# Performance work log

Hardware: AMD Instinct MI355X
Metric: run time of the kernel (lower is better)

## Reference

```python
import jax, jax.numpy as jnp
import numpy as np

N_NODES = 100000
N_EDGES = 1600000
D_IN, D_HID, D_OUT = 32, 64, 32


def gcn_conv(x, src, dst, W, b, n_nodes):
    """PyG-style GCNConv: x @ W, add self-loops, symmetric deg^-1/2 norm, scatter-add, + bias."""
    h = x @ W  # [N, d_out]
    ones = jnp.ones(src.shape[0], dtype=h.dtype)
    # in-degree at dst, +1 for the implicit self-loop
    deg = jax.ops.segment_sum(ones, dst, num_segments=n_nodes) + 1.0  # [N]
    dinv_sqrt = jax.lax.rsqrt(deg)
    norm = dinv_sqrt[src] * dinv_sqrt[dst]  # [E]
    agg = jax.ops.segment_sum(h[src] * norm[:, None], dst, num_segments=n_nodes)  # [N, d_out]
    agg = agg + h * (dinv_sqrt * dinv_sqrt)[:, None]  # self-loop term: deg^-1 * h_i
    return agg + b


def setup_inputs() -> dict:
    key = jax.random.key(0)
    ks = jax.random.split(key, 5)
    x = jax.random.normal(ks[0], (N_NODES, D_IN), dtype=jnp.float32)
    edge_index = jax.random.randint(ks[1], (2, N_EDGES), 0, N_NODES, dtype=jnp.int64)
    # Glorot-ish init for GCN weights
    W1 = jax.random.normal(ks[2], (D_IN, D_HID), dtype=jnp.float32) * (1.0 / np.sqrt(D_IN))
    b1 = jnp.zeros((D_HID,), dtype=jnp.float32)
    W2 = jax.random.normal(ks[3], (D_HID, D_OUT), dtype=jnp.float32) * (1.0 / np.sqrt(D_HID))
    b2 = jnp.zeros((D_OUT,), dtype=jnp.float32)
    return {"x": x, "edge_index": edge_index, "W1": W1, "b1": b1, "W2": W2, "b2": b2}


def reference(x, edge_index, W1, b1, W2, b2):
    src, dst = edge_index[0], edge_index[1]
    h = jax.nn.relu(gcn_conv(x, src, dst, W1, b1, N_NODES))
    h = gcn_conv(h, src, dst, W2, b2, N_NODES)
    # per-edge score: gather-multiply-sum
    logits = jnp.sum(h[src] * h[dst], axis=-1)  # [E]
    return logits
```

## Files before the change

kernel.cpp:

```cpp
#include <hip/hip_runtime.h>
#include <hip/hip_fp16.h>

#define N_NODES 100000
#define N_EDGES 1600000
#define D_IN 32
#define D_HID 64
#define D_OUT 32
#define CAP 48
#define PGROUPS 250
#define PGSIZE 400
#define PBINCAP 7200
#define PTILE 8192

__global__ void __launch_bounds__(512) partition_kernel(
    const int* __restrict__ src, const int* __restrict__ dst,
    int* __restrict__ gcur, int2* __restrict__ bins, int E) {
    __shared__ int lcnt[PGROUPS];
    __shared__ int lbase[PGROUPS];
    for (int t = threadIdx.x; t < PGROUPS; t += 512) lcnt[t] = 0;
    __syncthreads();
    int base = blockIdx.x * PTILE + threadIdx.x * 16;
    int s[16], d[16], g[16], p[16];
    int nloc = 0;
    if (base < E) nloc = min(16, E - base);
    if (nloc == 16) {
#pragma unroll
        for (int q = 0; q < 4; ++q) {
            int4 sv = *(const int4*)(src + base + 4 * q);
            int4 dv = *(const int4*)(dst + base + 4 * q);
            s[4*q+0] = sv.x; s[4*q+1] = sv.y; s[4*q+2] = sv.z; s[4*q+3] = sv.w;
            d[4*q+0] = dv.x; d[4*q+1] = dv.y; d[4*q+2] = dv.z; d[4*q+3] = dv.w;
        }
#pragma unroll
        for (int k = 0; k < 16; ++k) {
            g[k] = d[k] / PGSIZE;
            p[k] = atomicAdd(&lcnt[g[k]], 1);
        }
    } else {
        for (int k = 0; k < nloc; ++k) { s[k] = src[base + k]; d[k] = dst[base + k]; }
        for (int k = 0; k < nloc; ++k) {
            g[k] = d[k] / PGSIZE;
            p[k] = atomicAdd(&lcnt[g[k]], 1);
        }
    }
    __syncthreads();
    for (int t = threadIdx.x; t < PGROUPS; t += 512)
        lbase[t] = lcnt[t] ? atomicAdd(&gcur[t], lcnt[t]) : 0;
    __syncthreads();
    if (nloc == 16) {
#pragma unroll
        for (int k = 0; k < 16; ++k) {
            int idx = lbase[g[k]] + p[k];
            if (idx < PBINCAP) bins[(size_t)g[k] * PBINCAP + idx] = make_int2(s[k], d[k]);
        }
    } else {
        for (int k = 0; k < nloc; ++k) {
            int idx = lbase[g[k]] + p[k];
            if (idx < PBINCAP) bins[(size_t)g[k] * PBINCAP + idx] = make_int2(s[k], d[k]);
        }
    }
}

__global__ void __launch_bounds__(256) sort_scale_kernel(
    const int2* __restrict__ bins, const int* __restrict__ gcur,
    const float* __restrict__ x,
    int* __restrict__ cnt, int* __restrict__ csr, __half* __restrict__ xd) {
    __shared__ int lcnt[PGSIZE];
    int g = blockIdx.x;
    for (int t = threadIdx.x; t < PGSIZE; t += 256) lcnt[t] = 0;
    __syncthreads();
    int n = gcur[g];
    if (n > PBINCAP) n = PBINCAP;
    const int2* bin = bins + (size_t)g * PBINCAP;
    int lo = g * PGSIZE;
    int i = threadIdx.x;
    for (; i + 768 < n; i += 1024) {
        int2 e0 = bin[i];
        int2 e1 = bin[i + 256];
        int2 e2 = bin[i + 512];
        int2 e3 = bin[i + 768];
        int p0 = atomicAdd(&lcnt[e0.y - lo], 1);
        int p1 = atomicAdd(&lcnt[e1.y - lo], 1);
        int p2 = atomicAdd(&lcnt[e2.y - lo], 1);
        int p3 = atomicAdd(&lcnt[e3.y - lo], 1);
        if (p0 < CAP) csr[(size_t)e0.y * CAP + p0] = e0.x;
        if (p1 < CAP) csr[(size_t)e1.y * CAP + p1] = e1.x;
        if (p2 < CAP) csr[(size_t)e2.y * CAP + p2] = e2.x;
        if (p3 < CAP) csr[(size_t)e3.y * CAP + p3] = e3.x;
    }
    for (; i < n; i += 256) {
        int2 e = bin[i];
        int pos = atomicAdd(&lcnt[e.y - lo], 1);
        if (pos < CAP) csr[(size_t)e.y * CAP + pos] = e.x;
    }
    __syncthreads();
    for (int t = threadIdx.x; t < PGSIZE; t += 256) cnt[lo + t] = lcnt[t];
    for (int u = threadIdx.x; u < PGSIZE * 8; u += 256) {
        int t = u >> 3, c = (u & 7) * 4;
        int node = lo + t;
        float di = rsqrtf((float)lcnt[t] + 1.0f);
        float4 v = *(const float4*)(x + (size_t)node * D_IN + c);
        __half2 h0 = __floats2half2_rn(v.x * di, v.y * di);
        __half2 h1 = __floats2half2_rn(v.z * di, v.w * di);
        float2 packed = make_float2(*(float*)&h0, *(float*)&h1);
        *(float2*)(xd + (size_t)node * D_IN + c) = packed;
    }
}

#define ACC2(acc, raw) do { __half2* hp_ = (__half2*)&(raw); \
    float2 g0_ = __half22float2(hp_[0]), g1_ = __half22float2(hp_[1]); \
    (acc).x += g0_.x; (acc).y += g0_.y; (acc).z += g1_.x; (acc).w += g1_.y; } while (0)

__global__ void __launch_bounds__(256) agg1_kernel(
    const int* __restrict__ cnt, const int* __restrict__ csr,
    const __half* __restrict__ xd, float* __restrict__ axf, int N) {
    int gid = blockIdx.x * 256 + threadIdx.x;
    int n = gid >> 3;
    int c = (gid & 7) * 4;
    int cn = cnt[n];
    int m = cn < CAP ? cn : CAP;
    float di = rsqrtf((float)cn + 1.0f);

    float4 acc, accB = make_float4(0.f, 0.f, 0.f, 0.f);
    {
        float2 raw = *(const float2*)(xd + (size_t)n * D_IN + c);
        __half2* hp = (__half2*)&raw;
        float2 f0 = __half22float2(hp[0]), f1 = __half22float2(hp[1]);
        acc = make_float4(f0.x, f0.y, f1.x, f1.y);
    }
    const int4* row4 = (const int4*)(csr + (size_t)n * CAP);
    int i = 0;
    for (; i + 8 <= m; i += 8) {
        int4 sa = row4[(i >> 2) + 0];
        int4 sb = row4[(i >> 2) + 1];
        float2 r0 = *(const float2*)(xd + (size_t)sa.x * D_IN + c);
        float2 r1 = *(const float2*)(xd + (size_t)sa.y * D_IN + c);
        float2 r2 = *(const float2*)(xd + (size_t)sa.z * D_IN + c);
        float2 r3 = *(const float2*)(xd + (size_t)sa.w * D_IN + c);
        float2 r4 = *(const float2*)(xd + (size_t)sb.x * D_IN + c);
        float2 r5 = *(const float2*)(xd + (size_t)sb.y * D_IN + c);
        float2 r6 = *(const float2*)(xd + (size_t)sb.z * D_IN + c);
        float2 r7 = *(const float2*)(xd + (size_t)sb.w * D_IN + c);
        ACC2(acc, r0); ACC2(accB, r1); ACC2(acc, r2); ACC2(accB, r3);
        ACC2(acc, r4); ACC2(accB, r5); ACC2(acc, r6); ACC2(accB, r7);
    }
    for (; i + 4 <= m; i += 4) {
        int4 s4 = row4[i >> 2];
        float2 r0 = *(const float2*)(xd + (size_t)s4.x * D_IN + c);
        float2 r1 = *(const float2*)(xd + (size_t)s4.y * D_IN + c);
        float2 r2 = *(const float2*)(xd + (size_t)s4.z * D_IN + c);
        float2 r3 = *(const float2*)(xd + (size_t)s4.w * D_IN + c);
        ACC2(acc, r0); ACC2(accB, r1); ACC2(acc, r2); ACC2(accB, r3);
    }
    const int* row = csr + (size_t)n * CAP;
    for (; i < m; ++i) {
        float2 raw = *(const float2*)(xd + (size_t)row[i] * D_IN + c);
        ACC2(acc, raw);
    }
    float4 o = make_float4(di * (acc.x + accB.x), di * (acc.y + accB.y),
                           di * (acc.z + accB.z), di * (acc.w + accB.w));
    *(float4*)(axf + (size_t)n * D_IN + c) = o;
}

__global__ void __launch_bounds__(256) mlp_kernel(
    const int* __restrict__ cnt, const float* __restrict__ axf,
    const float* __restrict__ W1, const float* __restrict__ b1,
    const float* __restrict__ W2, __half* __restrict__ g2, int N) {
    __shared__ float W1s[D_IN * D_HID];
    __shared__ float W2s[D_HID * D_OUT];
    __shared__ float b1s[D_HID];
    __shared__ float axs[32][36];
    __shared__ float h1s[32][65];
    for (int t = threadIdx.x; t < D_IN * D_HID; t += 256) W1s[t] = W1[t];
    for (int t = threadIdx.x; t < D_HID * D_OUT; t += 256) W2s[t] = W2[t];
    if (threadIdx.x < D_HID) b1s[threadIdx.x] = b1[threadIdx.x];

    int nl = threadIdx.x >> 3;
    int l8 = threadIdx.x & 7;
    int n = blockIdx.x * 32 + nl;
    int c = l8 * 4;
    float di = rsqrtf((float)cnt[n] + 1.0f);
    float4 av = *(const float4*)(axf + (size_t)n * D_IN + c);
    *(float4*)&axs[nl][c] = av;
    __syncthreads();

#pragma unroll
    for (int jj = 0; jj < 8; ++jj) {
        int j = l8 * 8 + jj;
        float a = b1s[j];
#pragma unroll
        for (int k = 0; k < D_IN; ++k) a += axs[nl][k] * W1s[k * D_HID + j];
        h1s[nl][j] = fmaxf(a, 0.f);
    }
    __syncthreads();

    float o0 = 0.f, o1 = 0.f, o2 = 0.f, o3 = 0.f;
#pragma unroll
    for (int k = 0; k < D_HID; ++k) {
        float hk = h1s[nl][k];
        o0 += hk * W2s[k * D_OUT + c + 0];
        o1 += hk * W2s[k * D_OUT + c + 1];
        o2 += hk * W2s[k * D_OUT + c + 2];
        o3 += hk * W2s[k * D_OUT + c + 3];
    }
    __half2 p0 = __floats2half2_rn(di * o0, di * o1);
    __half2 p1 = __floats2half2_rn(di * o2, di * o3);
    float2 packed = make_float2(*(float*)&p0, *(float*)&p1);
    *(float2*)(g2 + (size_t)n * D_OUT + c) = packed;
}

__global__ void __launch_bounds__(256) agg2_kernel(
    const int* __restrict__ cnt, const int* __restrict__ csr,
    const __half* __restrict__ G, const float* __restrict__ b,
    __half* __restrict__ OUT, int N) {
    long long gid = (long long)blockIdx.x * blockDim.x + threadIdx.x;
    int n = (int)(gid >> 3);
    int c = ((int)gid & 7) * 4;
    if (n >= N) return;
    int cn = cnt[n];
    int m = cn < CAP ? cn : CAP;
    float4 acc, accB = make_float4(0.f, 0.f, 0.f, 0.f);
    {
        float2 raw = *(const float2*)(G + (long long)n * D_OUT + c);
        __half2* hp = (__half2*)&raw;
        float2 f0 = __half22float2(hp[0]), f1 = __half22float2(hp[1]);
        acc = make_float4(f0.x, f0.y, f1.x, f1.y);
    }
    const int4* row4 = (const int4*)(csr + (long long)n * CAP);
    int i = 0;
    for (; i + 8 <= m; i += 8) {
        int4 sa = row4[(i >> 2) + 0];
        int4 sb = row4[(i >> 2) + 1];
        float2 r0 = *(const float2*)(G + (long long)sa.x * D_OUT + c);
        float2 r1 = *(const float2*)(G + (long long)sa.y * D_OUT + c);
        float2 r2 = *(const float2*)(G + (long long)sa.z * D_OUT + c);
        float2 r3 = *(const float2*)(G + (long long)sa.w * D_OUT + c);
        float2 r4 = *(const float2*)(G + (long long)sb.x * D_OUT + c);
        float2 r5 = *(const float2*)(G + (long long)sb.y * D_OUT + c);
        float2 r6 = *(const float2*)(G + (long long)sb.z * D_OUT + c);
        float2 r7 = *(const float2*)(G + (long long)sb.w * D_OUT + c);
        ACC2(acc, r0); ACC2(accB, r1); ACC2(acc, r2); ACC2(accB, r3);
        ACC2(acc, r4); ACC2(accB, r5); ACC2(acc, r6); ACC2(accB, r7);
    }
    for (; i + 4 <= m; i += 4) {
        int4 s4 = row4[i >> 2];
        float2 r0 = *(const float2*)(G + (long long)s4.x * D_OUT + c);
        float2 r1 = *(const float2*)(G + (long long)s4.y * D_OUT + c);
        float2 r2 = *(const float2*)(G + (long long)s4.z * D_OUT + c);
        float2 r3 = *(const float2*)(G + (long long)s4.w * D_OUT + c);
        ACC2(acc, r0); ACC2(accB, r1); ACC2(acc, r2); ACC2(accB, r3);
    }
    const int* row = csr + (long long)n * CAP;
    for (; i < m; ++i) {
        float2 raw = *(const float2*)(G + (long long)row[i] * D_OUT + c);
        ACC2(acc, raw);
    }
    float di = rsqrtf((float)cn + 1.0f);
    __half2 h0 = __floats2half2_rn(di * (acc.x + accB.x) + b[c + 0],
                                   di * (acc.y + accB.y) + b[c + 1]);
    __half2 h1 = __floats2half2_rn(di * (acc.z + accB.z) + b[c + 2],
                                   di * (acc.w + accB.w) + b[c + 3]);
    float2 packed = make_float2(*(float*)&h0, *(float*)&h1);
    *(float2*)(OUT + (long long)n * D_OUT + c) = packed;
}

__global__ void logits_kernel(const int* __restrict__ src, const int* __restrict__ dst,
                              const __half* __restrict__ H, float* __restrict__ out, int E) {
    long long gid = (long long)blockIdx.x * blockDim.x + threadIdx.x;
    int e = (int)(gid >> 2);
    int c = ((int)gid & 3) * 8;
    if (e >= E) return;
    int s = src[e], d = dst[e];
    float4 ra = *(const float4*)(H + (long long)s * D_OUT + c);
    float4 rb = *(const float4*)(H + (long long)d * D_OUT + c);
    __half2* pa = (__half2*)&ra;
    __half2* pb = (__half2*)&rb;
    float p = 0.f;
#pragma unroll
    for (int k = 0; k < 4; ++k) {
        float2 fa = __half22float2(pa[k]);
        float2 fb = __half22float2(pb[k]);
        p += fa.x * fb.x + fa.y * fb.y;
    }
    p += __shfl_xor(p, 1);
    p += __shfl_xor(p, 2);
    if ((gid & 3) == 0) out[e] = p;
}

extern "C" void kernel_launch(void* const* d_in, const int* in_sizes, int n_in,
                              void* d_out, int out_size, void* d_ws, size_t ws_size,
                              hipStream_t stream) {
    const float* x  = (const float*)d_in[0];
    const int* edge = (const int*)d_in[1];
    const float* W1 = (const float*)d_in[2];
    const float* b1 = (const float*)d_in[3];
    const float* W2 = (const float*)d_in[4];
    const float* b2 = (const float*)d_in[5];
    float* out = (float*)d_out;

    const int* src = edge;
    const int* dst = edge + N_EDGES;

    char* ws = (char*)d_ws;
    int*    gcur = (int*)ws;
    int*    cnt  = gcur + 256;
    int*    csr  = cnt + N_NODES;
    int2*   bins = (int2*)(csr + (size_t)N_NODES * CAP);
    __half* xd   = (__half*)(bins + (size_t)PGROUPS * PBINCAP);
    float*  axf  = (float*)bins;
    __half* g2h  = xd;
    __half* h2h  = (__half*)bins;

    hipMemsetAsync(gcur, 0, 256 * sizeof(int), stream);

    partition_kernel<<<(N_EDGES + PTILE - 1) / PTILE, 512, 0, stream>>>(src, dst, gcur, bins, N_EDGES);

    sort_scale_kernel<<<PGROUPS, 256, 0, stream>>>(bins, gcur, x, cnt, csr, xd);

    agg1_kernel<<<(N_NODES * 8) / 256, 256, 0, stream>>>(cnt, csr, xd, axf, N_NODES);

    mlp_kernel<<<N_NODES / 32, 256, 0, stream>>>(cnt, axf, W1, b1, W2, g2h, N_NODES);

    agg2_kernel<<<(N_NODES * 8 + 255) / 256, 256, 0, stream>>>(cnt, csr, g2h, b2, h2h, N_NODES);

    logits_kernel<<<(N_EDGES * 4) / 256, 256, 0, stream>>>(src, dst, h2h, out, N_EDGES);
}
```

Baseline: 217.8 us.

## Split node feature tables into two 16-column planes processed in separate passes

Stores the scaled input features, hidden aggregates, layer-2 projections and final embeddings as two planes of 16 channels each instead of interleaved 32-channel rows. Each aggregation and the edge-logit kernel now run twice, once per plane, with the second logit pass accumulating into the output. The intent is to halve the working set each gather pass touches so it fits better in L2/MALL cache during random neighbor gathers. The cost is re-reading the CSR indices and edge lists twice, extra launches, and a read-modify-write of the output.

```diff
diff --git a/kernel.cpp b/kernel.cpp
--- a/kernel.cpp
+++ b/kernel.cpp
@@ -6,6 +6,7 @@
 #define D_IN 32
 #define D_HID 64
 #define D_OUT 32
+#define PL 16
 #define CAP 48
 #define PGROUPS 250
 #define PGSIZE 400
@@ -103,7 +104,8 @@
         __half2 h0 = __floats2half2_rn(v.x * di, v.y * di);
         __half2 h1 = __floats2half2_rn(v.z * di, v.w * di);
         float2 packed = make_float2(*(float*)&h0, *(float*)&h1);
-        *(float2*)(xd + (size_t)node * D_IN + c) = packed;
+        __half* xp = xd + (size_t)(c >> 4) * N_NODES * PL;
+        *(float2*)(xp + (size_t)node * PL + (c & 15)) = packed;
     }
 }
 
@@ -111,19 +113,20 @@
     float2 g0_ = __half22float2(hp_[0]), g1_ = __half22float2(hp_[1]); \
     (acc).x += g0_.x; (acc).y += g0_.y; (acc).z += g1_.x; (acc).w += g1_.y; } while (0)
 
-__global__ void __launch_bounds__(256) agg1_kernel(
+__global__ void __launch_bounds__(256) agg1_plane_kernel(
     const int* __restrict__ cnt, const int* __restrict__ csr,
-    const __half* __restrict__ xd, float* __restrict__ axf, int N) {
+    const __half* __restrict__ xdp, float* __restrict__ axfp, int N) {
     int gid = blockIdx.x * 256 + threadIdx.x;
-    int n = gid >> 3;
-    int c = (gid & 7) * 4;
+    int n = gid >> 2;
+    int c = (gid & 3) * 4;
+    if (n >= N) return;
     int cn = cnt[n];
     int m = cn < CAP ? cn : CAP;
     float di = rsqrtf((float)cn + 1.0f);
 
     float4 acc, accB = make_float4(0.f, 0.f, 0.f, 0.f);
     {
-        float2 raw = *(const float2*)(xd + (size_t)n * D_IN + c);
+        float2 raw = *(const float2*)(xdp + (size_t)n * PL + c);
         __half2* hp = (__half2*)&raw;
         float2 f0 = __half22float2(hp[0]), f1 = __half22float2(hp[1]);
         acc = make_float4(f0.x, f0.y, f1.x, f1.y);
@@ -133,33 +136,34 @@
     for (; i + 8 <= m; i += 8) {
         int4 sa = row4[(i >> 2) + 0];
         int4 sb = row4[(i >> 2) + 1];
-        float2 r0 = *(const float2*)(xd + (size_t)sa.x * D_IN + c);
-        float2 r1 = *(const float2*)(xd + (size_t)sa.y * D_IN + c);
-        float2 r2 = *(const float2*)(xd + (size_t)sa.z * D_IN + c);
-        float2 r3 = *(const float2*)(xd + (size_t)sa.w * D_IN + c);
-        float2 r4 = *(const float2*)(xd + (size_t)sb.x * D_IN + c);
-        float2 r5 = *(const float2*)(xd + (size_t)sb.y * D_IN + c);
-        float2 r6 = *(const float2*)(xd + (size_t)sb.z * D_IN + c);
-        float2 r7 = *(const float2*)(xd + (size_t)sb.w * D_IN + c);
+        float2 r0 = *(const float2*)(xdp + (size_t)sa.x * PL + c);
+        float2 r1 = *(const float2*)(xdp + (size_t)sa.y * PL + c);
+        float2 r2 = *(const float2*)(xdp + (size_t)sa.z * PL + c);
+        float2 r3 = *(const float2*)(xdp + (size_t)sa.w * PL + c);
+        float2 r4 = *(const float2*)(xdp + (size_t)sb.x * PL + c);
+        float2 r5 = *(const float2*)(xdp + (size_t)sb.y * PL + c);
+        float2 r6 = *(const float2*)(xdp + (size_t)sb.z * PL + c);
+        float2 r7 = *(const float2*)(xdp + (size_t)sb.w * PL + c);
         ACC2(acc, r0); ACC2(accB, r1); ACC2(acc, r2); ACC2(accB, r3);
         ACC2(acc, r4); ACC2(accB, r5); ACC2(acc, r6); ACC2(accB, r7);
     }
     for (; i + 4 <= m; i += 4) {
         int4 s4 = row4[i >> 2];
-        float2 r0 = *(const float2*)(xd + (size_t)s4.x * D_IN + c);
-        float2 r1 = *(const float2*)(xd + (size_t)s4.y * D_IN + c);
-        float2 r2 = *(const float2*)(xd + (size_t)s4.z * D_IN + c);
-        float2 r3 = *(const float2*)(xd + (size_t)s4.w * D_IN + c);
+        float2 r0 = *(const float2*)(xdp + (size_t)s4.x * PL + c);
+        float2 r1 = *(const float2*)(xdp + (size_t)s4.y * PL + c);
+        float2 r2 = *(const float2*)(xdp + (size_t)s4.z * PL + c);
+        float2 r3 = *(const float2*)(xdp + (size_t)s4.w * PL + c);
         ACC2(acc, r0); ACC2(accB, r1); ACC2(acc, r2); ACC2(accB, r3);
     }
     const int* row = csr + (size_t)n * CAP;
     for (; i < m; ++i) {
-        float2 raw = *(const float2*)(xd + (size_t)row[i] * D_IN + c);
+        int sv = row[i];
+        float2 raw = *(const float2*)(xdp + (size_t)sv * PL + c);
         ACC2(acc, raw);
     }
     float4 o = make_float4(di * (acc.x + accB.x), di * (acc.y + accB.y),
                            di * (acc.z + accB.z), di * (acc.w + accB.w));
-    *(float4*)(axf + (size_t)n * D_IN + c) = o;
+    *(float4*)(axfp + (size_t)n * PL + c) = o;
 }
 
 __global__ void __launch_bounds__(256) mlp_kernel(
@@ -180,7 +184,8 @@
     int n = blockIdx.x * 32 + nl;
     int c = l8 * 4;
     float di = rsqrtf((float)cnt[n] + 1.0f);
-    float4 av = *(const float4*)(axf + (size_t)n * D_IN + c);
+    const float* axp = axf + (size_t)(c >> 4) * N * PL;
+    float4 av = *(const float4*)(axp + (size_t)n * PL + (c & 15));
     *(float4*)&axs[nl][c] = av;
     __syncthreads();
 
@@ -206,85 +211,91 @@
     __half2 p0 = __floats2half2_rn(di * o0, di * o1);
     __half2 p1 = __floats2half2_rn(di * o2, di * o3);
     float2 packed = make_float2(*(float*)&p0, *(float*)&p1);
-    *(float2*)(g2 + (size_t)n * D_OUT + c) = packed;
-}
-
-__global__ void __launch_bounds__(256) agg2_kernel(
+    __half* gp = g2 + (size_t)(c >> 4) * N * PL;
+    *(float2*)(gp + (size_t)n * PL + (c & 15)) = packed;
+}
+
+__global__ void __launch_bounds__(256) agg2_plane_kernel(
     const int* __restrict__ cnt, const int* __restrict__ csr,
-    const __half* __restrict__ G, const float* __restrict__ b,
-    __half* __restrict__ OUT, int N) {
-    long long gid = (long long)blockIdx.x * blockDim.x + threadIdx.x;
-    int n = (int)(gid >> 3);
-    int c = ((int)gid & 7) * 4;
+    const __half* __restrict__ Gp, const float* __restrict__ bp,
+    __half* __restrict__ OUTp, int N) {
+    int gid = blockIdx.x * 256 + threadIdx.x;
+    int n = gid >> 2;
+    int c = (gid & 3) * 4;
     if (n >= N) return;
     int cn = cnt[n];
     int m = cn < CAP ? cn : CAP;
     float4 acc, accB = make_float4(0.f, 0.f, 0.f, 0.f);
     {
-        float2 raw = *(const float2*)(G + (long long)n * D_OUT + c);
+        float2 raw = *(const float2*)(Gp + (size_t)n * PL + c);
         __half2* hp = (__half2*)&raw;
         float2 f0 = __half22float2(hp[0]), f1 = __half22float2(hp[1]);
         acc = make_float4(f0.x, f0.y, f1.x, f1.y);
     }
-    const int4* row4 = (const int4*)(csr + (long long)n * CAP);
+    const int4* row4 = (const int4*)(csr + (size_t)n * CAP);
     int i = 0;
     for (; i + 8 <= m; i += 8) {
         int4 sa = row4[(i >> 2) + 0];
         int4 sb = row4[(i >> 2) + 1];
-        float2 r0 = *(const float2*)(G + (long long)sa.x * D_OUT + c);
-        float2 r1 = *(const float2*)(G + (long long)sa.y * D_OUT + c);
-        float2 r2 = *(const float2*)(G + (long long)sa.z * D_OUT + c);
-        float2 r3 = *(const float2*)(G + (long long)sa.w * D_OUT + c);
-        float2 r4 = *(const float2*)(G + (long long)sb.x * D_OUT + c);
-        float2 r5 = *(const float2*)(G + (long long)sb.y * D_OUT + c);
-        float2 r6 = *(const float2*)(G + (long long)sb.z * D_OUT + c);
-        float2 r7 = *(const float2*)(G + (long long)sb.w * D_OUT + c);
+        float2 r0 = *(const float2*)(Gp + (size_t)sa.x * PL + c);
+        float2 r1 = *(const float2*)(Gp + (size_t)sa.y * PL + c);
+        float2 r2 = *(const float2*)(Gp + (size_t)sa.z * PL + c);
+        float2 r3 = *(const float2*)(Gp + (size_t)sa.w * PL + c);
+        float2 r4 = *(const float2*)(Gp + (size_t)sb.x * PL + c);
+        float2 r5 = *(const float2*)(Gp + (size_t)sb.y * PL + c);
+        float2 r6 = *(const float2*)(Gp + (size_t)sb.z * PL + c);
+        float2 r7 = *(const float2*)(Gp + (size_t)sb.w * PL + c);
         ACC2(acc, r0); ACC2(accB, r1); ACC2(acc, r2); ACC2(accB, r3);
         ACC2(acc, r4); ACC2(accB, r5); ACC2(acc, r6); ACC2(accB, r7);
     }
     for (; i + 4 <= m; i += 4) {
         int4 s4 = row4[i >> 2];
-        float2 r0 = *(const float2*)(G + (long long)s4.x * D_OUT + c);
-        float2 r1 = *(const float2*)(G + (long long)s4.y * D_OUT + c);
-        float2 r2 = *(const float2*)(G + (long long)s4.z * D_OUT + c);
-        float2 r3 = *(const float2*)(G + (long long)s4.w * D_OUT + c);
+        float2 r0 = *(const float2*)(Gp + (size_t)s4.x * PL + c);
+        float2 r1 = *(const float2*)(Gp + (size_t)s4.y * PL + c);
+        float2 r2 = *(const float2*)(Gp + (size_t)s4.z * PL + c);
+        float2 r3 = *(const float2*)(Gp + (size_t)s4.w * PL + c);
         ACC2(acc, r0); ACC2(accB, r1); ACC2(acc, r2); ACC2(accB, r3);
     }
-    const int* row = csr + (long long)n * CAP;
+    const int* row = csr + (size_t)n * CAP;
     for (; i < m; ++i) {
-        float2 raw = *(const float2*)(G + (long long)row[i] * D_OUT + c);
+        int sv = row[i];
+        float2 raw = *(const float2*)(Gp + (size_t)sv * PL + c);
         ACC2(acc, raw);
     }
     float di = rsqrtf((float)cn + 1.0f);
-    __half2 h0 = __floats2half2_rn(di * (acc.x + accB.x) + b[c + 0],
-                                   di * (acc.y + accB.y) + b[c + 1]);
-    __half2 h1 = __floats2half2_rn(di * (acc.z + accB.z) + b[c + 2],
-                                   di * (acc.w + accB.w) + b[c + 3]);
+    __half2 h0 = __floats2half2_rn(di * (acc.x + accB.x) + bp[c + 0],
+                                   di * (acc.y + accB.y) + bp[c + 1]);
+    __half2 h1 = __floats2half2_rn(di * (acc.z + accB.z) + bp[c + 2],
+                                   di * (acc.w + accB.w) + bp[c + 3]);
     float2 packed = make_float2(*(float*)&h0, *(float*)&h1);
-    *(float2*)(OUT + (long long)n * D_OUT + c) = packed;
-}
-
-__global__ void logits_kernel(const int* __restrict__ src, const int* __restrict__ dst,
-                              const __half* __restrict__ H, float* __restrict__ out, int E) {
-    long long gid = (long long)blockIdx.x * blockDim.x + threadIdx.x;
-    int e = (int)(gid >> 2);
-    int c = ((int)gid & 3) * 8;
+    *(float2*)(OUTp + (size_t)n * PL + c) = packed;
+}
+
+__global__ void __launch_bounds__(256) logits_plane_kernel(
+    const int* __restrict__ src, const int* __restrict__ dst,
+    const __half* __restrict__ Hp, float* __restrict__ out, int E, int accum) {
+    int gid = blockIdx.x * 256 + threadIdx.x;
+    int e = gid >> 2;
+    int c = (gid & 3) * 4;
     if (e >= E) return;
     int s = src[e], d = dst[e];
-    float4 ra = *(const float4*)(H + (long long)s * D_OUT + c);
-    float4 rb = *(const float4*)(H + (long long)d * D_OUT + c);
+    float2 ra = *(const float2*)(Hp + (size_t)s * PL + c);
+    float2 rb = *(const float2*)(Hp + (size_t)d * PL + c);
     __half2* pa = (__half2*)&ra;
     __half2* pb = (__half2*)&rb;
     float p = 0.f;
 #pragma unroll
-    for (int k = 0; k < 4; ++k) {
+    for (int k = 0; k < 2; ++k) {
         float2 fa = __half22float2(pa[k]);
         float2 fb = __half22float2(pb[k]);
         p += fa.x * fb.x + fa.y * fb.y;
     }
     p += __shfl_xor(p, 1);
     p += __shfl_xor(p, 2);
-    if ((gid & 3) == 0) out[e] = p;
+    if ((gid & 3) == 0) {
+        if (accum) out[e] += p;
+        else       out[e]  = p;
+    }
 }
 
 extern "C" void kernel_launch(void* const* d_in, const int* in_sizes, int n_in,
@@ -308,8 +319,10 @@
     int2*   bins = (int2*)(csr + (size_t)N_NODES * CAP);
     __half* xd   = (__half*)(bins + (size_t)PGROUPS * PBINCAP);
     float*  axf  = (float*)bins;
-    __half* g2h  = xd;
-    __half* h2h  = (__half*)bins;
+    __half* g2   = xd;
+    __half* h2   = (__half*)bins;
+
+    const size_t PLN = (size_t)N_NODES * PL;
 
     hipMemsetAsync(gcur, 0, 256 * sizeof(int), stream);
 
@@ -317,11 +330,14 @@
 
     sort_scale_kernel<<<PGROUPS, 256, 0, stream>>>(bins, gcur, x, cnt, csr, xd);
 
-    agg1_kernel<<<(N_NODES * 8) / 256, 256, 0, stream>>>(cnt, csr, xd, axf, N_NODES);
-
-    mlp_kernel<<<N_NODES / 32, 256, 0, stream>>>(cnt, axf, W1, b1, W2, g2h, N_NODES);
-
-    agg2_kernel<<<(N_NODES * 8 + 255) / 256, 256, 0, stream>>>(cnt, csr, g2h, b2, h2h, N_NODES);
-
-    logits_kernel<<<(N_EDGES * 4) / 256, 256, 0, stream>>>(src, dst, h2h, out, N_EDGES);
-}
+    agg1_plane_kernel<<<(N_NODES * 4 + 255) / 256, 256, 0, stream>>>(cnt, csr, xd,       axf,       N_NODES);
+    agg1_plane_kernel<<<(N_NODES * 4 + 255) / 256, 256, 0, stream>>>(cnt, csr, xd + PLN, axf + PLN, N_NODES);
+
+    mlp_kernel<<<N_NODES / 32, 256, 0, stream>>>(cnt, axf, W1, b1, W2, g2, N_NODES);
+
+    agg2_plane_kernel<<<(N_NODES * 4 + 255) / 256, 256, 0, stream>>>(cnt, csr, g2,       b2,      h2,       N_NODES);
+    agg2_plane_kernel<<<(N_NODES * 4 + 255) / 256, 256, 0, stream>>>(cnt, csr, g2 + PLN, b2 + PL, h2 + PLN, N_NODES);
+
+    logits_plane_kernel<<<(N_EDGES * 4) / 256, 256, 0, stream>>>(src, dst, h2,       out, N_EDGES, 0);
+    logits_plane_kernel<<<(N_EDGES * 4) / 256, 256, 0, stream>>>(src, dst, h2 + PLN, out, N_EDGES, 1);
+}
```

After: 254.3 us. 16.8% more time.

## Fuse first-layer aggregation into MLP kernel and deepen gather unrolling

Applied to the files above, without the earlier changes.

The first-layer neighbor aggregation now runs inside the MLP kernel, writing aggregated features straight to shared memory. This removes the separate agg1 launch and the float32 round trip of the intermediate through global memory. Both gather loops also get a 16-wide unrolled stage to keep more loads in flight, which raises register pressure. Workspace buffers are remapped so g2h and h2h sit in the bins region, since xd must stay live.

```diff
diff --git a/kernel.cpp b/kernel.cpp
--- a/kernel.cpp
+++ b/kernel.cpp
@@ -111,59 +111,11 @@
     float2 g0_ = __half22float2(hp_[0]), g1_ = __half22float2(hp_[1]); \
     (acc).x += g0_.x; (acc).y += g0_.y; (acc).z += g1_.x; (acc).w += g1_.y; } while (0)
 
-__global__ void __launch_bounds__(256) agg1_kernel(
+#define GLD(tbl, idx, rv) float2 rv = *(const float2*)((tbl) + (size_t)(idx) * D_IN + c)
+
+__global__ void __launch_bounds__(256) agg_mlp_kernel(
     const int* __restrict__ cnt, const int* __restrict__ csr,
-    const __half* __restrict__ xd, float* __restrict__ axf, int N) {
-    int gid = blockIdx.x * 256 + threadIdx.x;
-    int n = gid >> 3;
-    int c = (gid & 7) * 4;
-    int cn = cnt[n];
-    int m = cn < CAP ? cn : CAP;
-    float di = rsqrtf((float)cn + 1.0f);
-
-    float4 acc, accB = make_float4(0.f, 0.f, 0.f, 0.f);
-    {
-        float2 raw = *(const float2*)(xd + (size_t)n * D_IN + c);
-        __half2* hp = (__half2*)&raw;
-        float2 f0 = __half22float2(hp[0]), f1 = __half22float2(hp[1]);
-        acc = make_float4(f0.x, f0.y, f1.x, f1.y);
-    }
-    const int4* row4 = (const int4*)(csr + (size_t)n * CAP);
-    int i = 0;
-    for (; i + 8 <= m; i += 8) {
-        int4 sa = row4[(i >> 2) + 0];
-        int4 sb = row4[(i >> 2) + 1];
-        float2 r0 = *(const float2*)(xd + (size_t)sa.x * D_IN + c);
-        float2 r1 = *(const float2*)(xd + (size_t)sa.y * D_IN + c);
-        float2 r2 = *(const float2*)(xd + (size_t)sa.z * D_IN + c);
-        float2 r3 = *(const float2*)(xd + (size_t)sa.w * D_IN + c);
-        float2 r4 = *(const float2*)(xd + (size_t)sb.x * D_IN + c);
-        float2 r5 = *(const float2*)(xd + (size_t)sb.y * D_IN + c);
-        float2 r6 = *(const float2*)(xd + (size_t)sb.z * D_IN + c);
-        float2 r7 = *(const float2*)(xd + (size_t)sb.w * D_IN + c);
-        ACC2(acc, r0); ACC2(accB, r1); ACC2(acc, r2); ACC2(accB, r3);
-        ACC2(acc, r4); ACC2(accB, r5); ACC2(acc, r6); ACC2(accB, r7);
-    }
-    for (; i + 4 <= m; i += 4) {
-        int4 s4 = row4[i >> 2];
-        float2 r0 = *(const float2*)(xd + (size_t)s4.x * D_IN + c);
-        float2 r1 = *(const float2*)(xd + (size_t)s4.y * D_IN + c);
-        float2 r2 = *(const float2*)(xd + (size_t)s4.z * D_IN + c);
-        float2 r3 = *(const float2*)(xd + (size_t)s4.w * D_IN + c);
-        ACC2(acc, r0); ACC2(accB, r1); ACC2(acc, r2); ACC2(accB, r3);
-    }
-    const int* row = csr + (size_t)n * CAP;
-    for (; i < m; ++i) {
-        float2 raw = *(const float2*)(xd + (size_t)row[i] * D_IN + c);
-        ACC2(acc, raw);
-    }
-    float4 o = make_float4(di * (acc.x + accB.x), di * (acc.y + accB.y),
-                           di * (acc.z + accB.z), di * (acc.w + accB.w));
-    *(float4*)(axf + (size_t)n * D_IN + c) = o;
-}
-
-__global__ void __launch_bounds__(256) mlp_kernel(
-    const int* __restrict__ cnt, const float* __restrict__ axf,
+    const __half* __restrict__ xd,
     const float* __restrict__ W1, const float* __restrict__ b1,
     const float* __restrict__ W2, __half* __restrict__ g2, int N) {
     __shared__ float W1s[D_IN * D_HID];
@@ -179,9 +131,53 @@
     int l8 = threadIdx.x & 7;
     int n = blockIdx.x * 32 + nl;
     int c = l8 * 4;
-    float di = rsqrtf((float)cnt[n] + 1.0f);
-    float4 av = *(const float4*)(axf + (size_t)n * D_IN + c);
-    *(float4*)&axs[nl][c] = av;
+    int cn = cnt[n];
+    int m = cn < CAP ? cn : CAP;
+    float di = rsqrtf((float)cn + 1.0f);
+
+    float4 acc, accB = make_float4(0.f, 0.f, 0.f, 0.f);
+    {
+        float2 raw = *(const float2*)(xd + (size_t)n * D_IN + c);
+        __half2* hp = (__half2*)&raw;
+        float2 f0 = __half22float2(hp[0]), f1 = __half22float2(hp[1]);
+        acc = make_float4(f0.x, f0.y, f1.x, f1.y);
+    }
+    const int4* row4 = (const int4*)(csr + (size_t)n * CAP);
+    int i = 0;
+    for (; i + 16 <= m; i += 16) {
+        int4 sa = row4[(i >> 2) + 0];
+        int4 sb = row4[(i >> 2) + 1];
+        int4 sc = row4[(i >> 2) + 2];
+        int4 sd = row4[(i >> 2) + 3];
+        GLD(xd, sa.x, r0);  GLD(xd, sa.y, r1);  GLD(xd, sa.z, r2);  GLD(xd, sa.w, r3);
+        GLD(xd, sb.x, r4);  GLD(xd, sb.y, r5);  GLD(xd, sb.z, r6);  GLD(xd, sb.w, r7);
+        GLD(xd, sc.x, r8);  GLD(xd, sc.y, r9);  GLD(xd, sc.z, r10); GLD(xd, sc.w, r11);
+        GLD(xd, sd.x, r12); GLD(xd, sd.y, r13); GLD(xd, sd.z, r14); GLD(xd, sd.w, r15);
+        ACC2(acc, r0);  ACC2(accB, r1);  ACC2(acc, r2);  ACC2(accB, r3);
+        ACC2(acc, r4);  ACC2(accB, r5);  ACC2(acc, r6);  ACC2(accB, r7);
+        ACC2(acc, r8);  ACC2(accB, r9);  ACC2(acc, r10); ACC2(accB, r11);
+        ACC2(acc, r12); ACC2(accB, r13); ACC2(acc, r14); ACC2(accB, r15);
+    }
+    for (; i + 8 <= m; i += 8) {
+        int4 sa = row4[(i >> 2) + 0];
+        int4 sb = row4[(i >> 2) + 1];
+        GLD(xd, sa.x, r0); GLD(xd, sa.y, r1); GLD(xd, sa.z, r2); GLD(xd, sa.w, r3);
+        GLD(xd, sb.x, r4); GLD(xd, sb.y, r5); GLD(xd, sb.z, r6); GLD(xd, sb.w, r7);
+        ACC2(acc, r0); ACC2(accB, r1); ACC2(acc, r2); ACC2(accB, r3);
+        ACC2(acc, r4); ACC2(accB, r5); ACC2(acc, r6); ACC2(accB, r7);
+    }
+    for (; i + 4 <= m; i += 4) {
+        int4 s4 = row4[i >> 2];
+        GLD(xd, s4.x, r0); GLD(xd, s4.y, r1); GLD(xd, s4.z, r2); GLD(xd, s4.w, r3);
+        ACC2(acc, r0); ACC2(accB, r1); ACC2(acc, r2); ACC2(accB, r3);
+    }
+    const int* row = csr + (size_t)n * CAP;
+    for (; i < m; ++i) {
+        float2 raw = *(const float2*)(xd + (size_t)row[i] * D_IN + c);
+        ACC2(acc, raw);
+    }
+    *(float4*)&axs[nl][c] = make_float4(di * (acc.x + accB.x), di * (acc.y + accB.y),
+                                        di * (acc.z + accB.z), di * (acc.w + accB.w));
     __syncthreads();
 
 #pragma unroll
@@ -213,46 +209,50 @@
     const int* __restrict__ cnt, const int* __restrict__ csr,
     const __half* __restrict__ G, const float* __restrict__ b,
     __half* __restrict__ OUT, int N) {
-    long long gid = (long long)blockIdx.x * blockDim.x + threadIdx.x;
-    int n = (int)(gid >> 3);
-    int c = ((int)gid & 7) * 4;
-    if (n >= N) return;
+    int gid = blockIdx.x * 256 + threadIdx.x;
+    int n = gid >> 3;
+    int c = (gid & 7) * 4;
     int cn = cnt[n];
     int m = cn < CAP ? cn : CAP;
     float4 acc, accB = make_float4(0.f, 0.f, 0.f, 0.f);
     {
-        float2 raw = *(const float2*)(G + (long long)n * D_OUT + c);
+        float2 raw = *(const float2*)(G + (size_t)n * D_OUT + c);
         __half2* hp = (__half2*)&raw;
         float2 f0 = __half22float2(hp[0]), f1 = __half22float2(hp[1]);
         acc = make_float4(f0.x, f0.y, f1.x, f1.y);
     }
-    const int4* row4 = (const int4*)(csr + (long long)n * CAP);
+    const int4* row4 = (const int4*)(csr + (size_t)n * CAP);
     int i = 0;
+    for (; i + 16 <= m; i += 16) {
+        int4 sa = row4[(i >> 2) + 0];
+        int4 sb = row4[(i >> 2) + 1];
+        int4 sc = row4[(i >> 2) + 2];
+        int4 sd = row4[(i >> 2) + 3];
+        GLD(G, sa.x, r0);  GLD(G, sa.y, r1);  GLD(G, sa.z, r2);  GLD(G, sa.w, r3);
+        GLD(G, sb.x, r4);  GLD(G, sb.y, r5);  GLD(G, sb.z, r6);  GLD(G, sb.w, r7);
+        GLD(G, sc.x, r8);  GLD(G, sc.y, r9);  GLD(G, sc.z, r10); GLD(G, sc.w, r11);
+        GLD(G, sd.x, r12); GLD(G, sd.y, r13); GLD(G, sd.z, r14); GLD(G, sd.w, r15);
+        ACC2(acc, r0);  ACC2(accB, r1);  ACC2(acc, r2);  ACC2(accB, r3);
+        ACC2(acc, r4);  ACC2(accB, r5);  ACC2(acc, r6);  ACC2(accB, r7);
+        ACC2(acc, r8);  ACC2(accB, r9);  ACC2(acc, r10); ACC2(accB, r11);
+        ACC2(acc, r12); ACC2(accB, r13); ACC2(acc, r14); ACC2(accB, r15);
+    }
     for (; i + 8 <= m; i += 8) {
         int4 sa = row4[(i >> 2) + 0];
         int4 sb = row4[(i >> 2) + 1];
-        float2 r0 = *(const float2*)(G + (long long)sa.x * D_OUT + c);
-        float2 r1 = *(const float2*)(G + (long long)sa.y * D_OUT + c);
-        float2 r2 = *(const float2*)(G + (long long)sa.z * D_OUT + c);
-        float2 r3 = *(const float2*)(G + (long long)sa.w * D_OUT + c);
-        float2 r4 = *(const float2*)(G + (long long)sb.x * D_OUT + c);
-        float2 r5 = *(const float2*)(G + (long long)sb.y * D_OUT + c);
-        float2 r6 = *(const float2*)(G + (long long)sb.z * D_OUT + c);
-        float2 r7 = *(const float2*)(G + (long long)sb.w * D_OUT + c);
+        GLD(G, sa.x, r0); GLD(G, sa.y, r1); GLD(G, sa.z, r2); GLD(G, sa.w, r3);
+        GLD(G, sb.x, r4); GLD(G, sb.y, r5); GLD(G, sb.z, r6); GLD(G, sb.w, r7);
         ACC2(acc, r0); ACC2(accB, r1); ACC2(acc, r2); ACC2(accB, r3);
         ACC2(acc, r4); ACC2(accB, r5); ACC2(acc, r6); ACC2(accB, r7);
     }
     for (; i + 4 <= m; i += 4) {
         int4 s4 = row4[i >> 2];
-        float2 r0 = *(const float2*)(G + (long long)s4.x * D_OUT + c);
-        float2 r1 = *(const float2*)(G + (long long)s4.y * D_OUT + c);
-        float2 r2 = *(const float2*)(G + (long long)s4.z * D_OUT + c);
-        float2 r3 = *(const float2*)(G + (long long)s4.w * D_OUT + c);
+        GLD(G, s4.x, r0); GLD(G, s4.y, r1); GLD(G, s4.z, r2); GLD(G, s4.w, r3);
         ACC2(acc, r0); ACC2(accB, r1); ACC2(acc, r2); ACC2(accB, r3);
     }
-    const int* row = csr + (long long)n * CAP;
+    const int* row = csr + (size_t)n * CAP;
     for (; i < m; ++i) {
-        float2 raw = *(const float2*)(G + (long long)row[i] * D_OUT + c);
+        float2 raw = *(const float2*)(G + (size_t)row[i] * D_IN + c);
         ACC2(acc, raw);
     }
     float di = rsqrtf((float)cn + 1.0f);
@@ -261,7 +261,7 @@
     __half2 h1 = __floats2half2_rn(di * (acc.z + accB.z) + b[c + 2],
                                    di * (acc.w + accB.w) + b[c + 3]);
     float2 packed = make_float2(*(float*)&h0, *(float*)&h1);
-    *(float2*)(OUT + (long long)n * D_OUT + c) = packed;
+    *(float2*)(OUT + (size_t)n * D_OUT + c) = packed;
 }
 
 __global__ void logits_kernel(const int* __restrict__ src, const int* __restrict__ dst,
@@ -307,9 +307,8 @@
     int*    csr  = cnt + N_NODES;
     int2*   bins = (int2*)(csr + (size_t)N_NODES * CAP);
     __half* xd   = (__half*)(bins + (size_t)PGROUPS * PBINCAP);
-    float*  axf  = (float*)bins;
-    __half* g2h  = xd;
-    __half* h2h  = (__half*)bins;
+    __half* g2h  = (__half*)bins;
+    __half* h2h  = g2h + (size_t)N_NODES * D_OUT;
 
     hipMemsetAsync(gcur, 0, 256 * sizeof(int), stream);
 
@@ -317,11 +316,9 @@
 
     sort_scale_kernel<<<PGROUPS, 256, 0, stream>>>(bins, gcur, x, cnt, csr, xd);
 
-    agg1_kernel<<<(N_NODES * 8) / 256, 256, 0, stream>>>(cnt, csr, xd, axf, N_NODES);
-
-    mlp_kernel<<<N_NODES / 32, 256, 0, stream>>>(cnt, axf, W1, b1, W2, g2h, N_NODES);
-
-    agg2_kernel<<<(N_NODES * 8 + 255) / 256, 256, 0, stream>>>(cnt, csr, g2h, b2, h2h, N_NODES);
+    agg_mlp_kernel<<<N_NODES / 32, 256, 0, stream>>>(cnt, csr, xd, W1, b1, W2, g2h, N_NODES);
+
+    agg2_kernel<<<(N_NODES * 8) / 256, 256, 0, stream>>>(cnt, csr, g2h, b2, h2h, N_NODES);
 
     logits_kernel<<<(N_EDGES * 4) / 256, 256, 0, stream>>>(src, dst, h2h, out, N_EDGES);
 }
```

New measurement: 211.1 us. -3.1%, faster.
